# Kernel tuning notes

Measured on AMD Instinct MI355X. Metric: run time of the kernel, lower is better.

## Reference

```python
import jax, jax.numpy as jnp
import numpy as np

PATCH = 8

def _to_patches(t):
    # [b,c,H,W] -> [b,c,H/8,W/8,8,8]
    b, c, H, W = t.shape
    t = t.reshape(b, c, H // PATCH, PATCH, W // PATCH, PATCH)
    return t.transpose(0, 1, 2, 4, 3, 5)

def _from_patches(t):
    # [b,c,h,w,8,8] -> [b,c,h*8,w*8]
    b, c, h, w, p1, p2 = t.shape
    return t.transpose(0, 1, 2, 4, 3, 5).reshape(b, c, h * p1, w * p2)

def setup_inputs() -> dict:
    key = jax.random.key(0)
    ks = jax.random.split(key, 8)
    dim = 64
    hid = dim * 6          # 384
    x = jax.random.normal(ks[0], (4, dim, 256, 256), dtype=jnp.float32)
    w_hidden = jax.random.normal(ks[1], (hid, dim), dtype=jnp.float32) * 0.05
    b_hidden = jax.random.normal(ks[2], (hid,), dtype=jnp.float32) * 0.02
    w_dw = jax.random.normal(ks[3], (hid, 3, 3), dtype=jnp.float32) * 0.1
    b_dw = jax.random.normal(ks[4], (hid,), dtype=jnp.float32) * 0.02
    w_proj = jax.random.normal(ks[5], (dim, dim * 2), dtype=jnp.float32) * 0.05
    b_proj = jax.random.normal(ks[6], (dim,), dtype=jnp.float32) * 0.02
    ln_w = jnp.ones((dim * 2,), dtype=jnp.float32)
    ln_b = jnp.zeros((dim * 2,), dtype=jnp.float32)
    return {"x": x, "w_hidden": w_hidden, "b_hidden": b_hidden,
            "w_dw": w_dw, "b_dw": b_dw, "w_proj": w_proj, "b_proj": b_proj,
            "ln_w": ln_w, "ln_b": ln_b}

def reference(x, w_hidden, b_hidden, w_dw, b_dw, w_proj, b_proj, ln_w, ln_b):
    # 1x1 conv: dim -> 6*dim
    hidden = jnp.einsum('bchw,oc->bohw', x, w_hidden) + b_hidden[None, :, None, None]
    # depthwise 3x3 conv, padding=1
    hid = hidden.shape[1]
    hidden = jax.lax.conv_general_dilated(
        hidden, w_dw[:, None, :, :], window_strides=(1, 1), padding='SAME',
        feature_group_count=hid,
        dimension_numbers=('NCHW', 'OIHW', 'NCHW')) + b_dw[None, :, None, None]
    q, k, v = jnp.split(hidden, 3, axis=1)  # each [b, 2*dim, H, W]
    # patch-wise circular convolution via rFFT over 8x8 patches
    q_fft = jnp.fft.rfft2(_to_patches(q))
    k_fft = jnp.fft.rfft2(_to_patches(k))
    out = jnp.fft.irfft2(q_fft * k_fft, s=(PATCH, PATCH))
    out = _from_patches(out).astype(x.dtype)
    # WithBias LayerNorm over channel dim (pixels are tokens, channels are features)
    mu = jnp.mean(out, axis=1, keepdims=True)
    var = jnp.var(out, axis=1, keepdims=True)
    out = (out - mu) / jnp.sqrt(var + 1e-5) * ln_w[None, :, None, None] + ln_b[None, :, None, None]
    output = v * out
    # 1x1 projection: 2*dim -> dim
    return jnp.einsum('bchw,oc->bohw', output, w_proj) + b_proj[None, :, None, None]
```

## Files before the change

### kernel.cpp

```cpp
#include <hip/hip_runtime.h>
#include <hip/hip_bf16.h>


typedef unsigned short ushort;
typedef __attribute__((ext_vector_type(8))) short short8;
typedef __attribute__((ext_vector_type(4))) float floatx4;
typedef __attribute__((ext_vector_type(2))) unsigned int uint2v;
typedef __attribute__((ext_vector_type(4))) unsigned int uint4v;

#define CC 64
#define HW 65536
#define QSU 68
#define TS 68
#define HS 68

#define WPT_OFF 0
#define WS_OFF 32768
#define WDWT_OFF 81920
#define XT_OFF  131072

__device__ __forceinline__ float bu2f(ushort u) {
    union { float f; unsigned i; } v; v.i = ((unsigned)u) << 16; return v.f;
}
__device__ __forceinline__ ushort f2bu(float f) {
    __hip_bfloat16 h = __float2bfloat16(f);
    return *(ushort*)&h;
}
__device__ __forceinline__ float ubits(unsigned u) {
    union { unsigned i; float f; } v; v.i = u; return v.f;
}
__device__ __forceinline__ void unpk(unsigned d, float& lo, float& hi) {
    lo = ubits(d << 16); hi = ubits(d & 0xffff0000u);
}

__global__ __launch_bounds__(256) void kx_tr(
    const float* __restrict__ x, ushort* __restrict__ XT) {
    int b = blockIdx.y;
    int hw = blockIdx.x * 256 + threadIdx.x;
    const float* xb = x + ((size_t)b * CC) * HW;
    ushort* XTb = XT + ((size_t)b * HW + hw) * 64;
#pragma unroll 2
    for (int c0 = 0; c0 < 64; c0 += 8) {
        ushort v[8];
#pragma unroll
        for (int j = 0; j < 8; j++)
            v[j] = f2bu(xb[(size_t)(c0 + j) * HW + hw]);
        *(short8*)(XTb + c0) = *(short8*)v;
    }
}

__global__ __launch_bounds__(256) void k0_prep(
    const float* __restrict__ wp, const float* __restrict__ wh,
    const float* __restrict__ wdw,
    float* __restrict__ wpT, ushort* __restrict__ WS, float* __restrict__ wdwT) {
    int t = threadIdx.x;
    for (int i = t; i < 8192; i += 256) {
        int c = i >> 6, o = i & 63;
        wpT[i] = wp[o * 128 + c];
    }
    for (int i = t; i < 24576; i += 256) {
        int j = i & 7;
        int lane = (i >> 3) & 63;
        int ks = (i >> 9) & 1;
        int mt = i >> 10;
        int o = mt * 16 + (lane & 15);
        int k = ks * 32 + ((lane >> 4) << 3) + j;
        WS[i] = f2bu(wh[o * 64 + k]);
    }
    for (int i = t; i < 3456; i += 256) {
        int k = i / 384, ch = i - k * 384;
        wdwT[i] = wdw[ch * 9 + k];
    }
}


__device__ __forceinline__ void load_afrags(short8 (&a)[4][2],
        const ushort* __restrict__ WSg, int ci, int lane) {
#pragma unroll
    for (int mt = 0; mt < 4; mt++) {
        int mtg = ci * 4 + mt;
#pragma unroll
        for (int ks = 0; ks < 2; ks++)
            a[mt][ks] = *(const short8*)(WSg + ((((mtg << 1) + ks) << 6) + lane) * 8);
    }
}

__device__ __forceinline__ void hid_mfma_store(
    ushort* halo_u, const short8 (&a)[4][2], const short8 (&bfr)[2][2],
    const bool (&img)[2], const bool (&live)[2], const int (&pxv)[2],
    const float* __restrict__ bh, int ci, int wave, int quad) {
#pragma unroll
    for (int s = 0; s < 2; s++) {
        if (wave + s * 4 > 6) continue;
        floatx4 acc[4];
#pragma unroll
        for (int mt = 0; mt < 4; mt++) {
            acc[mt] = (floatx4){0.f, 0.f, 0.f, 0.f};
            acc[mt] = __builtin_amdgcn_mfma_f32_16x16x32_bf16(a[mt][0], bfr[s][0], acc[mt], 0, 0, 0);
            acc[mt] = __builtin_amdgcn_mfma_f32_16x16x32_bf16(a[mt][1], bfr[s][1], acc[mt], 0, 0, 0);
        }
        int px = pxv[s];
#pragma unroll
        for (int mt = 0; mt < 4; mt++) {
            int chl = mt * 16 + quad * 4;
            float4 bv = *(const float4*)(bh + ci * 64 + chl);
            unsigned d0 = 0u, d1 = 0u;
            if (img[s]) {
                d0 = (unsigned)f2bu(acc[mt][0] + bv.x) | ((unsigned)f2bu(acc[mt][1] + bv.y) << 16);
                d1 = (unsigned)f2bu(acc[mt][2] + bv.z) | ((unsigned)f2bu(acc[mt][3] + bv.w) << 16);
            }
            if (live[s])
                *(uint2v*)(halo_u + px * HS + chl) = (uint2v){d0, d1};
        }
    }
}

__device__ __forceinline__ void dw_qk(const ushort* halo_u, ushort* dst,
        const float* __restrict__ wdwT, const float* __restrict__ bdw,
        int gcb, int rowbase, int tid) {
    int c2 = tid & 31, po = tid >> 5;
    int gch = gcb + c2 * 2;
    float w0[9], w1[9];
#pragma unroll
    for (int k = 0; k < 9; k++) {
        w0[k] = wdwT[k * 384 + gch];
        w1[k] = wdwT[k * 384 + gch + 1];
    }
    float b0 = bdw[gch], b1 = bdw[gch + 1];
    float a0[8], a1[8];
#pragma unroll
    for (int c = 0; c < 8; c++) { a0[c] = b0; a1[c] = b1; }
#pragma unroll
    for (int dr = 0; dr < 3; dr++) {
        int hb = (po + dr) * 10;
        float hx[10], hy[10];
#pragma unroll
        for (int i = 0; i < 10; i++) {
            unsigned d = *(const unsigned*)(halo_u + (hb + i) * HS + c2 * 2);
            unpk(d, hx[i], hy[i]);
        }
#pragma unroll
        for (int c = 0; c < 8; c++)
#pragma unroll
            for (int dc = 0; dc < 3; dc++) {
                a0[c] += w0[dr * 3 + dc] * hx[c + dc];
                a1[c] += w1[dr * 3 + dc] * hy[c + dc];
            }
    }
    ushort* r0p = dst + (rowbase + c2 * 2) * QSU + po * 8;
    ushort* r1p = r0p + QSU;
    unsigned p0 = (unsigned)f2bu(a0[0]) | ((unsigned)f2bu(a0[1]) << 16);
    unsigned p1 = (unsigned)f2bu(a0[2]) | ((unsigned)f2bu(a0[3]) << 16);
    unsigned p2 = (unsigned)f2bu(a0[4]) | ((unsigned)f2bu(a0[5]) << 16);
    unsigned p3 = (unsigned)f2bu(a0[6]) | ((unsigned)f2bu(a0[7]) << 16);
    *(uint2v*)(r0p) = (uint2v){p0, p1};
    *(uint2v*)(r0p + 4) = (uint2v){p2, p3};
    p0 = (unsigned)f2bu(a1[0]) | ((unsigned)f2bu(a1[1]) << 16);
    p1 = (unsigned)f2bu(a1[2]) | ((unsigned)f2bu(a1[3]) << 16);
    p2 = (unsigned)f2bu(a1[4]) | ((unsigned)f2bu(a1[5]) << 16);
    p3 = (unsigned)f2bu(a1[6]) | ((unsigned)f2bu(a1[7]) << 16);
    *(uint2v*)(r1p) = (uint2v){p0, p1};
    *(uint2v*)(r1p + 4) = (uint2v){p2, p3};
}

__device__ __forceinline__ void dw_v_apply(const ushort* halo_u, float* tb,
        const float* __restrict__ wdwT, const float* __restrict__ bdw,
        const float* __restrict__ lnw, const float* __restrict__ lnb,
        int gcb, int pix, int cj, float mu, float rsig) {
    int r = pix >> 3, cs = pix & 7;
    int ch0 = __builtin_amdgcn_readfirstlane(gcb + cj * 16);
    int ccs = ch0 - 256;
    float acc[16];
#pragma unroll
    for (int jj = 0; jj < 16; jj++) acc[jj] = bdw[ch0 + jj];
#pragma unroll
    for (int dr = 0; dr < 3; dr++) {
#pragma unroll
        for (int dc = 0; dc < 3; dc++) {
            int npx = (r + dr) * 10 + cs + dc;
            const ushort* hp = halo_u + npx * HS + cj * 16;
            uint2v d0 = *(const uint2v*)(hp);
            uint2v d1 = *(const uint2v*)(hp + 4);
            uint2v d2 = *(const uint2v*)(hp + 8);
            uint2v d3 = *(const uint2v*)(hp + 12);
            unsigned dd[8] = {d0.x, d0.y, d1.x, d1.y, d2.x, d2.y, d3.x, d3.y};
#pragma unroll
            for (int jj = 0; jj < 16; jj++) {
                unsigned u = dd[jj >> 1];
                float hv = (jj & 1) ? ubits(u & 0xffff0000u) : ubits(u << 16);
                acc[jj] += wdwT[(dr * 3 + dc) * 384 + ch0 + jj] * hv;
            }
        }
    }
#pragma unroll
    for (int jj = 0; jj < 16; jj++) {
        int cc = ccs + jj;
        float vv = bu2f(f2bu(acc[jj]));
        float tv = tb[cc * TS + pix];
        tb[cc * TS + pix] = ((tv - mu) * rsig * lnw[cc] + lnb[cc]) * vv;
    }
}

__global__ __launch_bounds__(256, 3) void k3_mega(
    const ushort* __restrict__ XT0, const ushort* __restrict__ WSg,
    const float* __restrict__ bh, const float* __restrict__ wpTg,
    const float* __restrict__ bp, const float* __restrict__ lnw,
    const float* __restrict__ lnb, const float* __restrict__ wdwT,
    const float* __restrict__ bdw, float* __restrict__ out) {
    __shared__ float SH[12800];
    ushort* qb_u = (ushort*)SH;
    ushort* kb_u = (ushort*)SH + 8704;
    float* tb = SH;
    float* red = SH + 8704;
    ushort* halo_u = (ushort*)SH + 18432;
    float* wpc = SH + 8704;

    int tid = threadIdx.x;
    int lane = tid & 63, wave = tid >> 6;
    int lane15 = lane & 15, quad = lane >> 4;
    int b = blockIdx.y;
    const ushort* XT = XT0 + (size_t)b * HW * 64;
    int bid = blockIdx.x;
    int p = ((bid & 7) << 7) | (bid >> 3);
    int prow = p >> 5, pcol = p & 31;
    int r0 = prow * 8, c0 = pcol * 8;

    short8 bfr[2][2];
    bool img[2], live[2];
    int pxv[2];
#pragma unroll
    for (int s = 0; s < 2; s++) {
        int nt = wave + s * 4;
        int px = nt * 16 + lane15;
        pxv[s] = px;
        live[s] = (nt <= 6) && (px < 100);
        int hr = px / 10, hc = px - hr * 10;
        int gr = r0 - 1 + hr, gc = c0 - 1 + hc;
        img[s] = live[s] && ((unsigned)gr < 256u) && ((unsigned)gc < 256u);
        size_t gidx = img[s] ? (size_t)(gr * 256 + gc) * 64 : 0;
        short8 z = (short8){0, 0, 0, 0, 0, 0, 0, 0};
        short8 t0 = *(const short8*)(XT + gidx + quad * 8);
        short8 t1 = *(const short8*)(XT + gidx + 32 + quad * 8);
        bfr[s][0] = img[s] ? t0 : z;
        bfr[s][1] = img[s] ? t1 : z;
    }

    short8 aA[4][2], aB[4][2];
    load_afrags(aA, WSg, 0, lane);
#pragma unroll
    for (int ci = 0; ci < 4; ci++) {
        if (ci) __syncthreads();
        hid_mfma_store(halo_u, aA, bfr, img, live, pxv, bh, ci, wave, quad);
        load_afrags(aB, WSg, ci + 1, lane);
        __syncthreads();
        dw_qk(halo_u, (ci < 2 ? qb_u : kb_u), wdwT, bdw, ci * 64, (ci & 1) * 64, tid);
#pragma unroll
        for (int mt = 0; mt < 4; mt++)
#pragma unroll
            for (int ks = 0; ks < 2; ks++) aA[mt][ks] = aB[mt][ks];
    }
    __syncthreads();

    int c = tid >> 1, h = tid & 1;
    float qr[64];
    {
        const ushort* qrow = qb_u + c * QSU;
#pragma unroll
        for (int j = 0; j < 16; j++) {
            uint2v d = *(const uint2v*)(qrow + 4 * j);
            unpk(d.x, qr[4 * j], qr[4 * j + 1]);
            unpk(d.y, qr[4 * j + 2], qr[4 * j + 3]);
        }
    }
    float acc[8][4];
#pragma unroll
    for (int r = 0; r < 8; r++)
#pragma unroll
        for (int sc = 0; sc < 4; sc++) acc[r][sc] = 0.f;
    {
        const ushort* krow = kb_u + c * QSU;
#pragma unroll 2
        for (int m = 0; m < 8; m++) {
            float kr[8];
#pragma unroll
            for (int u2 = 0; u2 < 4; u2++) {
                int colo = (u2 * 2 + 4 * h) & 7;
                unsigned d = *(const unsigned*)(krow + m * 8 + colo);
                unpk(d, kr[u2 * 2], kr[u2 * 2 + 1]);
            }
#pragma unroll
            for (int r = 0; r < 8; r++) {
                int i = (r - m) & 7;
#pragma unroll
                for (int sc = 0; sc < 4; sc++)
#pragma unroll
                    for (int j = 0; j < 8; j++)
                        acc[r][sc] += qr[i * 8 + j] * kr[(sc - j) & 7];
            }
        }
    }
    __syncthreads();

#pragma unroll
    for (int r = 0; r < 8; r++) {
        float4 v = {acc[r][0], acc[r][1], acc[r][2], acc[r][3]};
        *(float4*)(tb + c * TS + r * 8 + h * 4) = v;
    }
    hid_mfma_store(halo_u, aA, bfr, img, live, pxv, bh, 4, wave, quad);
    load_afrags(aB, WSg, 5, lane);
    __syncthreads();

    int pix = tid & 63, cg = tid >> 6;
    float sum = 0.f, sq = 0.f;
#pragma unroll
    for (int j = 0; j < 32; j++) {
        int cc = cg * 32 + j;
        float v = tb[cc * TS + pix];
        sum += v; sq += v * v;
    }
    red[cg * 64 + pix] = sum;
    red[256 + cg * 64 + pix] = sq;
    __syncthreads();
    float ts = red[pix] + red[64 + pix] + red[128 + pix] + red[192 + pix];
    float tq = red[256 + pix] + red[320 + pix] + red[384 + pix] + red[448 + pix];
    float mu = ts * (1.f / 128.f);
    float var = tq * (1.f / 128.f) - mu * mu;
    float rsig = rsqrtf(var + 1e-5f);

    dw_v_apply(halo_u, tb, wdwT, bdw, lnw, lnb, 256, pix, cg, mu, rsig);
    __syncthreads();
    hid_mfma_store(halo_u, aB, bfr, img, live, pxv, bh, 5, wave, quad);
    __syncthreads();
    dw_v_apply(halo_u, tb, wdwT, bdw, lnw, lnb, 320, pix, cg, mu, rsig);
    __syncthreads();

#pragma unroll
    for (int j = 0; j < 4; j++)
        ((float4*)wpc)[j * 256 + tid] = ((const float4*)wpTg)[j * 256 + tid];
    __syncthreads();

    int oi = tid & 15, pg = tid >> 4;
    int o0 = oi * 4, pix0 = pg * 4;
    float pe[4][4];
#pragma unroll
    for (int oo = 0; oo < 4; oo++) {
        float bbv = bp[o0 + oo];
#pragma unroll
        for (int pp = 0; pp < 4; pp++) pe[oo][pp] = bbv;
    }
#pragma unroll 4
    for (int cc = 0; cc < 64; cc++) {
        float4 wv = *(const float4*)(wpc + cc * 64 + o0);
        float4 tv = *(const float4*)(tb + cc * TS + pix0);
        pe[0][0] += wv.x * tv.x; pe[0][1] += wv.x * tv.y; pe[0][2] += wv.x * tv.z; pe[0][3] += wv.x * tv.w;
        pe[1][0] += wv.y * tv.x; pe[1][1] += wv.y * tv.y; pe[1][2] += wv.y * tv.z; pe[1][3] += wv.y * tv.w;
        pe[2][0] += wv.z * tv.x; pe[2][1] += wv.z * tv.y; pe[2][2] += wv.z * tv.z; pe[2][3] += wv.z * tv.w;
        pe[3][0] += wv.w * tv.x; pe[3][1] += wv.w * tv.y; pe[3][2] += wv.w * tv.z; pe[3][3] += wv.w * tv.w;
    }
    __syncthreads();
#pragma unroll
    for (int j = 0; j < 4; j++)
        ((float4*)wpc)[j * 256 + tid] = ((const float4*)wpTg)[1024 + j * 256 + tid];
    __syncthreads();
#pragma unroll 4
    for (int cc = 0; cc < 64; cc++) {
        float4 wv = *(const float4*)(wpc + cc * 64 + o0);
        float4 tv = *(const float4*)(tb + (64 + cc) * TS + pix0);
        pe[0][0] += wv.x * tv.x; pe[0][1] += wv.x * tv.y; pe[0][2] += wv.x * tv.z; pe[0][3] += wv.x * tv.w;
        pe[1][0] += wv.y * tv.x; pe[1][1] += wv.y * tv.y; pe[1][2] += wv.y * tv.z; pe[1][3] += wv.y * tv.w;
        pe[2][0] += wv.z * tv.x; pe[2][1] += wv.z * tv.y; pe[2][2] += wv.z * tv.z; pe[2][3] += wv.z * tv.w;
        pe[3][0] += wv.w * tv.x; pe[3][1] += wv.w * tv.y; pe[3][2] += wv.w * tv.z; pe[3][3] += wv.w * tv.w;
    }
    int row = (prow << 3) + (pix0 >> 3);
    int col = (pcol << 3) + (pix0 & 7);
#pragma unroll
    for (int oo = 0; oo < 4; oo++) {
        float4 v = {pe[oo][0], pe[oo][1], pe[oo][2], pe[oo][3]};
        *(float4*)(out + (((size_t)(b * CC + o0 + oo)) << 16) + row * 256 + col) = v;
    }
}

extern "C" void kernel_launch(void* const* d_in, const int* in_sizes, int n_in,
                              void* d_out, int out_size, void* d_ws, size_t ws_size,
                              hipStream_t stream) {
    (void)in_sizes; (void)n_in; (void)out_size; (void)ws_size;
    const float* x   = (const float*)d_in[0];
    const float* wh  = (const float*)d_in[1];
    const float* bh  = (const float*)d_in[2];
    const float* wdw = (const float*)d_in[3];
    const float* bdw = (const float*)d_in[4];
    const float* wp  = (const float*)d_in[5];
    const float* bp  = (const float*)d_in[6];
    const float* lnw = (const float*)d_in[7];
    const float* lnb = (const float*)d_in[8];
    float* out = (float*)d_out;

    char* ws = (char*)d_ws;
    float* wpT = (float*)(ws + WPT_OFF);
    ushort* WS = (ushort*)(ws + WS_OFF);
    float* wdwT = (float*)(ws + WDWT_OFF);
    ushort* XT = (ushort*)(ws + XT_OFF);

    kx_tr<<<dim3(256, 4), dim3(256), 0, stream>>>(x, XT);
    k0_prep<<<dim3(1), dim3(256), 0, stream>>>(wp, wh, wdw, wpT, WS, wdwT);
    k3_mega<<<dim3(1024, 4), dim3(256), 0, stream>>>(
        XT, WS, bh, wpT, bp, lnw, lnb, wdwT, bdw, out);
}
```

Before: 503.2 us.

## Run output projection on bf16 MFMA with hi/lo split and staged transpose

The final 128->64 projection moves from fp32 FMA loops in shared memory onto bf16 MFMA instructions. To keep accuracy close to fp32, both weights and activations are split into high and low bf16 parts, giving three MFMAs per tile. Results are written patch-major to a workspace buffer, and a new transpose kernel scatters them into NCHW order. The weight-prep kernel now also runs on more blocks. This cuts the per-block ALU work but adds an extra full-output round trip through global memory and an extra launch, and the transpose kernel's per-thread stores are strided by a full channel plane.

```diff
diff --git a/kernel.cpp b/kernel.cpp
--- a/kernel.cpp
+++ b/kernel.cpp
@@ -13,11 +13,16 @@
 #define QSU 68
 #define TS 68
 #define HS 68
-
-#define WPT_OFF 0
+#define TBS 136
+#define OSS 68
+
+#define WPSH_OFF 0
+#define WPSL_OFF 16384
 #define WS_OFF 32768
 #define WDWT_OFF 81920
 #define XT_OFF  131072
+#define XT_BYTES (4ull * HW * 64 * 2)
+#define OUTT_OFF (XT_OFF + XT_BYTES)
 
 __device__ __forceinline__ float bu2f(ushort u) {
     union { float f; unsigned i; } v; v.i = ((unsigned)u) << 16; return v.f;
@@ -52,13 +57,22 @@
 __global__ __launch_bounds__(256) void k0_prep(
     const float* __restrict__ wp, const float* __restrict__ wh,
     const float* __restrict__ wdw,
-    float* __restrict__ wpT, ushort* __restrict__ WS, float* __restrict__ wdwT) {
-    int t = threadIdx.x;
-    for (int i = t; i < 8192; i += 256) {
-        int c = i >> 6, o = i & 63;
-        wpT[i] = wp[o * 128 + c];
-    }
-    for (int i = t; i < 24576; i += 256) {
+    ushort* __restrict__ WPSH, ushort* __restrict__ WPSL,
+    ushort* __restrict__ WS, float* __restrict__ wdwT) {
+    int t0 = blockIdx.x * 256 + threadIdx.x;
+    for (int i = t0; i < 8192; i += 4096) {
+        int j = i & 7;
+        int lane = (i >> 3) & 63;
+        int ks = (i >> 9) & 3;
+        int mt = i >> 11;
+        int o = mt * 16 + (lane & 15);
+        int cc = ks * 32 + ((lane >> 4) << 3) + j;
+        float w = wp[o * 128 + cc];
+        ushort hi = f2bu(w);
+        WPSH[i] = hi;
+        WPSL[i] = f2bu(w - bu2f(hi));
+    }
+    for (int i = t0; i < 24576; i += 4096) {
         int j = i & 7;
         int lane = (i >> 3) & 63;
         int ks = (i >> 9) & 1;
@@ -67,7 +81,7 @@
         int k = ks * 32 + ((lane >> 4) << 3) + j;
         WS[i] = f2bu(wh[o * 64 + k]);
     }
-    for (int i = t; i < 3456; i += 256) {
+    for (int i = t0; i < 3456; i += 4096) {
         int k = i / 384, ch = i - k * 384;
         wdwT[i] = wdw[ch * 9 + k];
     }
@@ -163,10 +177,10 @@
     *(uint2v*)(r1p + 4) = (uint2v){p2, p3};
 }
 
-__device__ __forceinline__ void dw_v_apply(const ushort* halo_u, float* tb,
+__device__ __forceinline__ void dw_v_collect(const ushort* halo_u, const float* tb,
         const float* __restrict__ wdwT, const float* __restrict__ bdw,
         const float* __restrict__ lnw, const float* __restrict__ lnb,
-        int gcb, int pix, int cj, float mu, float rsig) {
+        int gcb, int pix, int cj, float mu, float rsig, float (&tp)[16]) {
     int r = pix >> 3, cs = pix & 7;
     int ch0 = __builtin_amdgcn_readfirstlane(gcb + cj * 16);
     int ccs = ch0 - 256;
@@ -197,23 +211,41 @@
         int cc = ccs + jj;
         float vv = bu2f(f2bu(acc[jj]));
         float tv = tb[cc * TS + pix];
-        tb[cc * TS + pix] = ((tv - mu) * rsig * lnw[cc] + lnb[cc]) * vv;
-    }
+        tp[jj] = ((tv - mu) * rsig * lnw[cc] + lnb[cc]) * vv;
+    }
+}
+
+__device__ __forceinline__ void split_store(ushort* tBh, ushort* tBl,
+        const float (&tp)[16], int pix, int colbase) {
+    ushort hi[16], lo[16];
+#pragma unroll
+    for (int jj = 0; jj < 16; jj++) {
+        ushort h = f2bu(tp[jj]);
+        hi[jj] = h;
+        lo[jj] = f2bu(tp[jj] - bu2f(h));
+    }
+    *(short8*)(tBh + pix * TBS + colbase) = *(short8*)hi;
+    *(short8*)(tBh + pix * TBS + colbase + 8) = *(short8*)(hi + 8);
+    *(short8*)(tBl + pix * TBS + colbase) = *(short8*)lo;
+    *(short8*)(tBl + pix * TBS + colbase + 8) = *(short8*)(lo + 8);
 }
 
 __global__ __launch_bounds__(256, 3) void k3_mega(
     const ushort* __restrict__ XT0, const ushort* __restrict__ WSg,
-    const float* __restrict__ bh, const float* __restrict__ wpTg,
+    const float* __restrict__ bh,
+    const ushort* __restrict__ WPSH, const ushort* __restrict__ WPSL,
     const float* __restrict__ bp, const float* __restrict__ lnw,
     const float* __restrict__ lnb, const float* __restrict__ wdwT,
-    const float* __restrict__ bdw, float* __restrict__ out) {
+    const float* __restrict__ bdw, float* __restrict__ outT) {
     __shared__ float SH[12800];
     ushort* qb_u = (ushort*)SH;
     ushort* kb_u = (ushort*)SH + 8704;
     float* tb = SH;
     float* red = SH + 8704;
     ushort* halo_u = (ushort*)SH + 18432;
-    float* wpc = SH + 8704;
+    ushort* tBh = (ushort*)SH;
+    ushort* tBl = (ushort*)SH + 8704;
+    float* outS = SH;
 
     int tid = threadIdx.x;
     int lane = tid & 63, wave = tid >> 6;
@@ -327,56 +359,85 @@
     float var = tq * (1.f / 128.f) - mu * mu;
     float rsig = rsqrtf(var + 1e-5f);
 
-    dw_v_apply(halo_u, tb, wdwT, bdw, lnw, lnb, 256, pix, cg, mu, rsig);
+    float tpA[16], tpB[16];
+    dw_v_collect(halo_u, tb, wdwT, bdw, lnw, lnb, 256, pix, cg, mu, rsig, tpA);
     __syncthreads();
     hid_mfma_store(halo_u, aB, bfr, img, live, pxv, bh, 5, wave, quad);
     __syncthreads();
-    dw_v_apply(halo_u, tb, wdwT, bdw, lnw, lnb, 320, pix, cg, mu, rsig);
-    __syncthreads();
-
-#pragma unroll
-    for (int j = 0; j < 4; j++)
-        ((float4*)wpc)[j * 256 + tid] = ((const float4*)wpTg)[j * 256 + tid];
-    __syncthreads();
-
-    int oi = tid & 15, pg = tid >> 4;
-    int o0 = oi * 4, pix0 = pg * 4;
-    float pe[4][4];
-#pragma unroll
-    for (int oo = 0; oo < 4; oo++) {
-        float bbv = bp[o0 + oo];
-#pragma unroll
-        for (int pp = 0; pp < 4; pp++) pe[oo][pp] = bbv;
-    }
-#pragma unroll 4
-    for (int cc = 0; cc < 64; cc++) {
-        float4 wv = *(const float4*)(wpc + cc * 64 + o0);
-        float4 tv = *(const float4*)(tb + cc * TS + pix0);
-        pe[0][0] += wv.x * tv.x; pe[0][1] += wv.x * tv.y; pe[0][2] += wv.x * tv.z; pe[0][3] += wv.x * tv.w;
-        pe[1][0] += wv.y * tv.x; pe[1][1] += wv.y * tv.y; pe[1][2] += wv.y * tv.z; pe[1][3] += wv.y * tv.w;
-        pe[2][0] += wv.z * tv.x; pe[2][1] += wv.z * tv.y; pe[2][2] += wv.z * tv.z; pe[2][3] += wv.z * tv.w;
-        pe[3][0] += wv.w * tv.x; pe[3][1] += wv.w * tv.y; pe[3][2] += wv.w * tv.z; pe[3][3] += wv.w * tv.w;
-    }
-    __syncthreads();
-#pragma unroll
-    for (int j = 0; j < 4; j++)
-        ((float4*)wpc)[j * 256 + tid] = ((const float4*)wpTg)[1024 + j * 256 + tid];
-    __syncthreads();
-#pragma unroll 4
-    for (int cc = 0; cc < 64; cc++) {
-        float4 wv = *(const float4*)(wpc + cc * 64 + o0);
-        float4 tv = *(const float4*)(tb + (64 + cc) * TS + pix0);
-        pe[0][0] += wv.x * tv.x; pe[0][1] += wv.x * tv.y; pe[0][2] += wv.x * tv.z; pe[0][3] += wv.x * tv.w;
-        pe[1][0] += wv.y * tv.x; pe[1][1] += wv.y * tv.y; pe[1][2] += wv.y * tv.z; pe[1][3] += wv.y * tv.w;
-        pe[2][0] += wv.z * tv.x; pe[2][1] += wv.z * tv.y; pe[2][2] += wv.z * tv.z; pe[2][3] += wv.z * tv.w;
-        pe[3][0] += wv.w * tv.x; pe[3][1] += wv.w * tv.y; pe[3][2] += wv.w * tv.z; pe[3][3] += wv.w * tv.w;
-    }
-    int row = (prow << 3) + (pix0 >> 3);
-    int col = (pcol << 3) + (pix0 & 7);
-#pragma unroll
-    for (int oo = 0; oo < 4; oo++) {
-        float4 v = {pe[oo][0], pe[oo][1], pe[oo][2], pe[oo][3]};
-        *(float4*)(out + (((size_t)(b * CC + o0 + oo)) << 16) + row * 256 + col) = v;
+    dw_v_collect(halo_u, tb, wdwT, bdw, lnw, lnb, 320, pix, cg, mu, rsig, tpB);
+    __syncthreads();
+
+    split_store(tBh, tBl, tpA, pix, cg * 16);
+    split_store(tBh, tBl, tpB, pix, 64 + cg * 16);
+    __syncthreads();
+
+    short8 bhf[4], blf[4];
+#pragma unroll
+    for (int ks = 0; ks < 4; ks++) {
+        const int rb = (wave * 16 + lane15) * TBS + ks * 32 + quad * 8;
+        bhf[ks] = *(const short8*)(tBh + rb);
+        blf[ks] = *(const short8*)(tBl + rb);
+    }
+    floatx4 pacc[4];
+#pragma unroll
+    for (int mt = 0; mt < 4; mt++) {
+        float4 bv = *(const float4*)(bp + mt * 16 + quad * 4);
+        pacc[mt] = (floatx4){bv.x, bv.y, bv.z, bv.w};
+    }
+#pragma unroll
+    for (int mt = 0; mt < 4; mt++) {
+#pragma unroll
+        for (int ks = 0; ks < 4; ks++) {
+            short8 ah = *(const short8*)(WPSH + (((mt * 4 + ks) << 6) + lane) * 8);
+            short8 al = *(const short8*)(WPSL + (((mt * 4 + ks) << 6) + lane) * 8);
+            pacc[mt] = __builtin_amdgcn_mfma_f32_16x16x32_bf16(ah, bhf[ks], pacc[mt], 0, 0, 0);
+            pacc[mt] = __builtin_amdgcn_mfma_f32_16x16x32_bf16(ah, blf[ks], pacc[mt], 0, 0, 0);
+            pacc[mt] = __builtin_amdgcn_mfma_f32_16x16x32_bf16(al, bhf[ks], pacc[mt], 0, 0, 0);
+        }
+    }
+    __syncthreads();
+
+#pragma unroll
+    for (int mt = 0; mt < 4; mt++) {
+        float4 v = {pacc[mt][0], pacc[mt][1], pacc[mt][2], pacc[mt][3]};
+        *(float4*)(outS + (wave * 16 + lane15) * OSS + mt * 16 + quad * 4) = v;
+    }
+    __syncthreads();
+    {
+        int px = tid >> 2, oq = (tid & 3) * 16;
+        float* g = outT + ((size_t)(b * 1024 + p) * 64 + px) * 64 + oq;
+        const float* srow = outS + px * OSS + oq;
+#pragma unroll
+        for (int k = 0; k < 4; k++)
+            *(float4*)(g + k * 4) = *(const float4*)(srow + k * 4);
+    }
+}
+
+__global__ __launch_bounds__(256) void k4_tr(
+    const float* __restrict__ outT, float* __restrict__ out) {
+    int b = blockIdx.y;
+    int xb = blockIdx.x;
+    int pr = xb >> 1, half = xb & 1;
+    int tid = threadIdx.x;
+    int c128 = tid & 127, rr = tid >> 7;
+    int col = half * 128 + c128;
+    int p = pr * 32 + (col >> 3);
+    int cs = col & 7;
+    const float* tbase = outT + (size_t)(b * 1024 + p) * 4096;
+    float* obase = out + ((size_t)b * 64) * 65536 + col;
+#pragma unroll
+    for (int r4 = 0; r4 < 4; r4++) {
+        int r = rr * 4 + r4;
+        int px = r * 8 + cs;
+        const float* src = tbase + (size_t)px * 64;
+        float v[64];
+#pragma unroll
+        for (int k = 0; k < 16; k++)
+            *(float4*)(v + k * 4) = *(const float4*)(src + k * 4);
+        float* dst = obase + (size_t)(pr * 8 + r) * 256;
+#pragma unroll
+        for (int o = 0; o < 64; o++)
+            dst[(size_t)o * 65536] = v[o];
     }
 }
 
@@ -396,13 +457,16 @@
     float* out = (float*)d_out;
 
     char* ws = (char*)d_ws;
-    float* wpT = (float*)(ws + WPT_OFF);
+    ushort* WPSH = (ushort*)(ws + WPSH_OFF);
+    ushort* WPSL = (ushort*)(ws + WPSL_OFF);
     ushort* WS = (ushort*)(ws + WS_OFF);
     float* wdwT = (float*)(ws + WDWT_OFF);
     ushort* XT = (ushort*)(ws + XT_OFF);
+    float* outT = (float*)(ws + OUTT_OFF);
 
     kx_tr<<<dim3(256, 4), dim3(256), 0, stream>>>(x, XT);
-    k0_prep<<<dim3(1), dim3(256), 0, stream>>>(wp, wh, wdw, wpT, WS, wdwT);
+    k0_prep<<<dim3(16), dim3(256), 0, stream>>>(wp, wh, wdw, WPSH, WPSL, WS, wdwT);
     k3_mega<<<dim3(1024, 4), dim3(256), 0, stream>>>(
-        XT, WS, bh, wpT, bp, lnw, lnb, wdwT, bdw, out);
-}
+        XT, WS, bh, WPSH, WPSL, bp, lnw, lnb, wdwT, bdw, outT);
+    k4_tr<<<dim3(64, 4), dim3(256), 0, stream>>>(outT, out);
+}
```

Result: slower. 525.3 us (+4.4%).
